# Kernel tuning notes

Hardware: AMD Instinct MI355X
Metric: run time of the kernel (lower is better)

## Reference

```python
import jax, jax.numpy as jnp
import numpy as np

B, S, D = 1024, 48, 256   # graphs, nodes-per-graph, embedding dim (= input_dim)
GDIM = 512                # graph_dim
N = B * S                 # total nodes
E = 4 * N                 # directed edges (avg degree ~4, molecular graphs)
W_SCALE = 0.05


def setup_inputs() -> dict:
    key = jax.random.key(0)
    ks = jax.random.split(key, 8)
    return {
        "sub2gene_out": jax.random.normal(ks[0], (B, S, D), jnp.float32),
        "edge_index": jax.random.randint(ks[1], (2, E), 0, N, dtype=jnp.int64),
        # conv1: in_channels = 2*D (concat of x and laplacian-smoothed x)
        "W_l1": jax.random.normal(ks[2], (GDIM, 2 * D), jnp.float32) * W_SCALE,
        "W_r1": jax.random.normal(ks[3], (GDIM, 2 * D), jnp.float32) * W_SCALE,
        "b1": jnp.zeros((GDIM,), jnp.float32),
        # conv2: graph_dim -> graph_dim
        "W_l2": jax.random.normal(ks[4], (GDIM, GDIM), jnp.float32) * W_SCALE,
        "W_r2": jax.random.normal(ks[5], (GDIM, GDIM), jnp.float32) * W_SCALE,
        "b2": jnp.zeros((GDIM,), jnp.float32),
    }


def sage_conv(x, src, dst, W_l, W_r, b, n):
    """PyG SAGEConv (mean aggregation, root_weight=True):
    out_i = W_l @ mean_{j in N(i)} x_j + W_r @ x_i + b, messages flow src->dst."""
    msg = x[src]                                            # [E, F] gather
    agg = jax.ops.segment_sum(msg, dst, num_segments=n)     # [N, F]
    cnt = jax.ops.segment_sum(jnp.ones((src.shape[0],), x.dtype), dst, num_segments=n)
    mean = agg / jnp.maximum(cnt, 1.0)[:, None]
    return mean @ W_l.T + x @ W_r.T + b


def reference(sub2gene_out, edge_index, W_l1, W_r1, b1, W_l2, W_r2, b2):
    b_, s_, d_ = sub2gene_out.shape
    n = b_ * s_
    x = sub2gene_out.reshape(n, d_)                         # cat of per-graph node features
    row, col = edge_index[0], edge_index[1]

    # sym-normalized Laplacian L = I - D^{-1/2} A D^{-1/2}; lap_x = L @ x
    ones_e = jnp.ones((row.shape[0],), x.dtype)
    deg = jax.ops.segment_sum(ones_e, row, num_segments=n)
    dinv = jnp.where(deg > 0, 1.0, 0.0) / jnp.sqrt(jnp.maximum(deg, 1.0))
    w = -(dinv[row] * dinv[col])                            # off-diagonal -A_norm
    lap_x = x + jax.ops.segment_sum(w[:, None] * x[col], row, num_segments=n)

    x_comb = jnp.concatenate([x, lap_x], axis=-1)           # [N, 2D]
    h = jax.nn.gelu(sage_conv(x_comb, row, col, W_l1, W_r1, b1, n), approximate=False)
    h = sage_conv(h, row, col, W_l2, W_r2, b2, n)           # [N, GDIM]

    # global_mean_pool: every graph has exactly s_ nodes
    batch = jnp.repeat(jnp.arange(b_), s_)
    pooled = jax.ops.segment_sum(h, batch, num_segments=b_) / jnp.asarray(s_, h.dtype)
    return pooled                                           # [B, GDIM]
```

## Files before the change

### kernel.cpp

```cpp
#include <hip/hip_runtime.h>
#include <math.h>

typedef unsigned short u16;
typedef __attribute__((ext_vector_type(8))) short bf16x8;
typedef __attribute__((ext_vector_type(4))) float f32x4;

#define NB 1024
#define NS 48
#define ND 256
#define NN (NB*NS)
#define NE (4*NN)
#define GD 512

__device__ __forceinline__ void gld16(const void* g, void* l) {
  __builtin_amdgcn_global_load_lds(
      (const __attribute__((address_space(1))) void*)(void*)g,
      (__attribute__((address_space(3))) void*)l, 16, 0, 0);
}

__device__ __forceinline__ float bf2f(u16 h) {
  unsigned u = ((unsigned)h) << 16; float f; __builtin_memcpy(&f, &u, 4); return f;
}
__device__ __forceinline__ u16 f2bf(float f) {
  unsigned u; __builtin_memcpy(&u, &f, 4);
  u += 0x7fffu + ((u >> 16) & 1u);
  return (u16)(u >> 16);
}
__device__ __forceinline__ void unpack8(uint4 v, float* f) {
  f[0]=bf2f((u16)(v.x & 0xffff)); f[1]=bf2f((u16)(v.x >> 16));
  f[2]=bf2f((u16)(v.y & 0xffff)); f[3]=bf2f((u16)(v.y >> 16));
  f[4]=bf2f((u16)(v.z & 0xffff)); f[5]=bf2f((u16)(v.z >> 16));
  f[6]=bf2f((u16)(v.w & 0xffff)); f[7]=bf2f((u16)(v.w >> 16));
}
__device__ __forceinline__ uint4 pack8(const float* f) {
  uint4 v;
  v.x = (unsigned)f2bf(f[0]) | ((unsigned)f2bf(f[1]) << 16);
  v.y = (unsigned)f2bf(f[2]) | ((unsigned)f2bf(f[3]) << 16);
  v.z = (unsigned)f2bf(f[4]) | ((unsigned)f2bf(f[5]) << 16);
  v.w = (unsigned)f2bf(f[6]) | ((unsigned)f2bf(f[7]) << 16);
  return v;
}


__global__ void k_hist(const int* __restrict__ ei, int* __restrict__ deg, int* __restrict__ cnt) {
  int e = blockIdx.x * 256 + threadIdx.x;
  if (e < NE) {
    atomicAdd(&deg[ei[e]], 1);
    atomicAdd(&cnt[ei[NE + e]], 1);
  }
}

__global__ void k_exscan2(const int* __restrict__ deg, const int* __restrict__ cnt,
                          int* __restrict__ rowOff, int* __restrict__ colOff,
                          float* __restrict__ dinv) {
  const int t = threadIdx.x;
  const int base = t * 48;
  if (blockIdx.x == 2) {
    for (int i = 0; i < 48; ++i) {
      int d = deg[base + i];
      dinv[base + i] = (d > 0) ? rsqrtf((float)d) : 0.0f;
    }
    return;
  }
  __shared__ int sums[1024];
  const int* in = blockIdx.x ? cnt : deg;
  int* out = blockIdx.x ? colOff : rowOff;
  int s = 0;
  for (int i = 0; i < 48; ++i) s += in[base + i];
  sums[t] = s;
  __syncthreads();
  for (int off = 1; off < 1024; off <<= 1) {
    int v = (t >= off) ? sums[t - off] : 0;
    __syncthreads();
    sums[t] += v;
    __syncthreads();
  }
  int run = (t == 0) ? 0 : sums[t - 1];
  for (int i = 0; i < 48; ++i) { int v = in[base + i]; out[base + i] = run; run += v; }
  if (t == 1023) out[NN] = run;
}

__global__ void k_fill(const int* __restrict__ ei,
                       const int* __restrict__ rowOff, const int* __restrict__ colOff,
                       int* __restrict__ rowFill, int* __restrict__ colFill,
                       int* __restrict__ rowCol, int* __restrict__ colSrc) {
  int e = blockIdx.x * 256 + threadIdx.x;
  if (e < NE) {
    int r = ei[e], c = ei[NE + e];
    int pr = atomicAdd(&rowFill[r], 1);
    rowCol[rowOff[r] + pr] = c;
    int pc = atomicAdd(&colFill[c], 1);
    colSrc[colOff[c] + pc] = r;
  }
}

__global__ void k_wx(const float* __restrict__ Wr1, const float* __restrict__ Wl1,
                     const float* __restrict__ Wr2, const float* __restrict__ Wl2,
                     u16* __restrict__ Wc, const float* __restrict__ x, u16* __restrict__ xb) {
  if (blockIdx.x < 1024) {
    int i = (blockIdx.x * 256 + threadIdx.x) * 4;
    int which = i >> 18;
    int off = i & 262143;
    const float* W = (which == 0) ? Wr1 : (which == 1) ? Wl1 : (which == 2) ? Wr2 : Wl2;
    float4 v = *(const float4*)(W + off);
    ushort4 h; h.x = f2bf(v.x); h.y = f2bf(v.y); h.z = f2bf(v.z); h.w = f2bf(v.w);
    *(ushort4*)(Wc + i) = h;
  } else {
    int i = ((blockIdx.x - 1024) * 256 + threadIdx.x) * 8;
    float4 v0 = *(const float4*)(x + i);
    float4 v1 = *(const float4*)(x + i + 4);
    float f[8] = {v0.x, v0.y, v0.z, v0.w, v1.x, v1.y, v1.z, v1.w};
    *(uint4*)(xb + i) = pack8(f);
  }
}

__global__ void k_lap(const u16* __restrict__ xb, const int* __restrict__ rowOff,
                      const int* __restrict__ rowCol, const float* __restrict__ dinv,
                      u16* __restrict__ xc) {
  const int gid = blockIdx.x * 256 + threadIdx.x;
  const int wid = gid >> 6, lane = gid & 63;
  const int node = wid * 2 + (lane >> 5);
  const int f0 = (lane & 31) * 8;
  float xi[8]; unpack8(*(const uint4*)(xb + (size_t)node * ND + f0), xi);
  float a[8] = {};
  const int s0 = rowOff[node], s1 = rowOff[node + 1];
  for (int p = s0; p < s1; p += 4) {
    const int q1 = (p + 1 < s1) ? p + 1 : s1 - 1;
    const int q2 = (p + 2 < s1) ? p + 2 : s1 - 1;
    const int q3 = (p + 3 < s1) ? p + 3 : s1 - 1;
    const int c0 = rowCol[p], c1 = rowCol[q1], c2 = rowCol[q2], c3 = rowCol[q3];
    const float w0 = dinv[c0];
    const float w1 = (p + 1 < s1) ? dinv[c1] : 0.f;
    const float w2 = (p + 2 < s1) ? dinv[c2] : 0.f;
    const float w3 = (p + 3 < s1) ? dinv[c3] : 0.f;
    float g0[8], g1[8], g2[8], g3[8];
    unpack8(*(const uint4*)(xb + (size_t)c0 * ND + f0), g0);
    unpack8(*(const uint4*)(xb + (size_t)c1 * ND + f0), g1);
    unpack8(*(const uint4*)(xb + (size_t)c2 * ND + f0), g2);
    unpack8(*(const uint4*)(xb + (size_t)c3 * ND + f0), g3);
    #pragma unroll
    for (int j = 0; j < 8; ++j) a[j] += w0 * g0[j] + w1 * g1[j] + w2 * g2[j] + w3 * g3[j];
  }
  const float di = dinv[node];
  u16* dst = xc + (size_t)node * GD + f0;
  *(uint4*)dst = pack8(xi);
  float l[8];
  #pragma unroll
  for (int j = 0; j < 8; ++j) l[j] = xi[j] - di * a[j];
  *(uint4*)(dst + ND) = pack8(l);
}

__global__ void k_aggx(const u16* __restrict__ xc, const int* __restrict__ colOff,
                       const int* __restrict__ colSrc, u16* __restrict__ xagg) {
  const int gid = blockIdx.x * 256 + threadIdx.x;
  const int node = gid >> 6, lane = gid & 63;
  const int f0 = lane * 8;
  float acc[8] = {};
  const int s0 = colOff[node], s1 = colOff[node + 1];
  for (int p = s0; p < s1; p += 4) {
    const int q1 = (p + 1 < s1) ? p + 1 : s1 - 1;
    const int q2 = (p + 2 < s1) ? p + 2 : s1 - 1;
    const int q3 = (p + 3 < s1) ? p + 3 : s1 - 1;
    const int c0 = colSrc[p], c1 = colSrc[q1], c2 = colSrc[q2], c3 = colSrc[q3];
    const float w1 = (p + 1 < s1) ? 1.f : 0.f;
    const float w2 = (p + 2 < s1) ? 1.f : 0.f;
    const float w3 = (p + 3 < s1) ? 1.f : 0.f;
    float g0[8], g1[8], g2[8], g3[8];
    unpack8(*(const uint4*)(xc + (size_t)c0 * GD + f0), g0);
    unpack8(*(const uint4*)(xc + (size_t)c1 * GD + f0), g1);
    unpack8(*(const uint4*)(xc + (size_t)c2 * GD + f0), g2);
    unpack8(*(const uint4*)(xc + (size_t)c3 * GD + f0), g3);
    #pragma unroll
    for (int j = 0; j < 8; ++j) acc[j] += g0[j] + w1 * g1[j] + w2 * g2[j] + w3 * g3[j];
  }
  const float inv = (s1 > s0) ? 1.0f / (float)(s1 - s0) : 1.0f;
  float res[8];
  #pragma unroll
  for (int j = 0; j < 8; ++j) res[j] = acc[j] * inv;
  *(uint4*)(xagg + (size_t)node * GD + f0) = pack8(res);
}

template <int MODE>
__global__ __launch_bounds__(256) void k_gemm(const u16* __restrict__ A0,
                                              const u16* __restrict__ A1,
                                              const u16* __restrict__ B0,
                                              const u16* __restrict__ B1,
                                              const float* __restrict__ bias,
                                              void* __restrict__ OutP) {
  __shared__ u16 As[128 * 32];
  __shared__ u16 Bs[128 * 32];
  const int tid = threadIdx.x;
  const int w = tid >> 6, lane = tid & 63;
  const int wr = w >> 1, wc = w & 1;

  const int cpx = gridDim.x >> 3;
  const int o = blockIdx.x;
  const int swz = (o & 7) * cpx + (o >> 3);
  const int bx = swz >> 2;
  const int by = swz & 3;

  const int c0 = w * 2, c1 = c0 + 1;
  const int lrow = lane >> 2;
  const int lcol = ((lane & 3) ^ ((lane >> 3) & 3)) * 8;
  const size_t a0r = (size_t)(bx * 128 + c0 * 16 + lrow) * GD + lcol;
  const size_t a1r = (size_t)(bx * 128 + c1 * 16 + lrow) * GD + lcol;
  const size_t b0r = (size_t)(by * 128 + c0 * 16 + lrow) * GD + lcol;
  const size_t b1r = (size_t)(by * 128 + c1 * 16 + lrow) * GD + lcol;
  u16* As0 = As + c0 * 512; u16* As1 = As + c1 * 512;
  u16* Bs0 = Bs + c0 * 512; u16* Bs1 = Bs + c1 * 512;

  const int kslot = ((lane >> 4) ^ ((lane >> 1) & 3)) * 8;
  const int aoff = (wr * 64 + (lane & 15)) * 32 + kslot;
  const int boff = (wc * 64 + (lane & 15)) * 32 + kslot;

  f32x4 acc[4][4] = {};

  #pragma unroll
  for (int half = 0; half < 2; ++half) {
    const u16* Ab = half ? A1 : A0;
    const u16* Bb = half ? B1 : B0;
    for (int kt = 0; kt < 512; kt += 32) {
      gld16(Ab + kt + a0r, As0);
      gld16(Ab + kt + a1r, As1);
      gld16(Bb + kt + b0r, Bs0);
      gld16(Bb + kt + b1r, Bs1);
      __syncthreads();
      bf16x8 aF[4], bF[4];
      #pragma unroll
      for (int i = 0; i < 4; ++i) aF[i] = *(const bf16x8*)(As + aoff + i * 512);
      #pragma unroll
      for (int i = 0; i < 4; ++i) bF[i] = *(const bf16x8*)(Bs + boff + i * 512);
      #pragma unroll
      for (int mi = 0; mi < 4; ++mi)
        #pragma unroll
        for (int ni = 0; ni < 4; ++ni)
          acc[mi][ni] = __builtin_amdgcn_mfma_f32_16x16x32_bf16(aF[mi], bF[ni], acc[mi][ni], 0, 0, 0);
      __syncthreads();
    }
  }

  const int lc = lane & 15, lr = (lane >> 4) * 4;
  const size_t r0 = (size_t)bx * 128 + wr * 64;
  const int cb = by * 128 + wc * 64;
  float bv[4];
  #pragma unroll
  for (int ni = 0; ni < 4; ++ni) bv[ni] = bias[cb + ni * 16 + lc];
  #pragma unroll
  for (int mi = 0; mi < 4; ++mi)
    #pragma unroll
    for (int ni = 0; ni < 4; ++ni)
      #pragma unroll
      for (int r = 0; r < 4; ++r) {
        float v = acc[mi][ni][r] + bv[ni];
        const size_t idx = (r0 + mi * 16 + lr + r) * GD + (cb + ni * 16 + lc);
        if (MODE == 0) {
          v = 0.5f * v * (1.0f + erff(v * 0.70710678118654752f));
          ((u16*)OutP)[idx] = f2bf(v);
        } else {
          ((float*)OutP)[idx] = v;
        }
      }
}

__global__ __launch_bounds__(256) void k_aggh(const u16* __restrict__ h, const int* __restrict__ colOff,
                                              const int* __restrict__ colSrc,
                                              u16* __restrict__ hrb, u16* __restrict__ hab) {
  __shared__ float red[2][4][GD];
  const int g = blockIdx.x;
  const int t = threadIdx.x, w = t >> 6, lane = t & 63;
  const int f0 = lane * 8;
  float pr[8] = {}, pa[8] = {};
  for (int n = w; n < NS; n += 4) {
    const int node = g * NS + n;
    float tmp[8];
    unpack8(*(const uint4*)(h + (size_t)node * GD + f0), tmp);
    #pragma unroll
    for (int j = 0; j < 8; ++j) pr[j] += tmp[j];
    float acc[8] = {};
    const int s0 = colOff[node], s1 = colOff[node + 1];
    for (int p = s0; p < s1; p += 4) {
      const int q1 = (p + 1 < s1) ? p + 1 : s1 - 1;
      const int q2 = (p + 2 < s1) ? p + 2 : s1 - 1;
      const int q3 = (p + 3 < s1) ? p + 3 : s1 - 1;
      const int c0 = colSrc[p], c1 = colSrc[q1], c2 = colSrc[q2], c3 = colSrc[q3];
      const float w1 = (p + 1 < s1) ? 1.f : 0.f;
      const float w2 = (p + 2 < s1) ? 1.f : 0.f;
      const float w3 = (p + 3 < s1) ? 1.f : 0.f;
      float g0[8], g1[8], g2[8], g3[8];
      unpack8(*(const uint4*)(h + (size_t)c0 * GD + f0), g0);
      unpack8(*(const uint4*)(h + (size_t)c1 * GD + f0), g1);
      unpack8(*(const uint4*)(h + (size_t)c2 * GD + f0), g2);
      unpack8(*(const uint4*)(h + (size_t)c3 * GD + f0), g3);
      #pragma unroll
      for (int j = 0; j < 8; ++j) acc[j] += g0[j] + w1 * g1[j] + w2 * g2[j] + w3 * g3[j];
    }
    const float inv = (s1 > s0) ? 1.0f / (float)(s1 - s0) : 1.0f;
    #pragma unroll
    for (int j = 0; j < 8; ++j) pa[j] += acc[j] * inv;
  }
  #pragma unroll
  for (int j = 0; j < 8; ++j) { red[0][w][f0 + j] = pr[j]; red[1][w][f0 + j] = pa[j]; }
  __syncthreads();
  const int f = t * 2;
  const float invS = 1.0f / (float)NS;
  float r0 = (red[0][0][f] + red[0][1][f] + red[0][2][f] + red[0][3][f]) * invS;
  float r1 = (red[0][0][f+1] + red[0][1][f+1] + red[0][2][f+1] + red[0][3][f+1]) * invS;
  float a0 = (red[1][0][f] + red[1][1][f] + red[1][2][f] + red[1][3][f]) * invS;
  float a1 = (red[1][0][f+1] + red[1][1][f+1] + red[1][2][f+1] + red[1][3][f+1]) * invS;
  *(unsigned*)(hrb + (size_t)g * GD + f) = (unsigned)f2bf(r0) | ((unsigned)f2bf(r1) << 16);
  *(unsigned*)(hab + (size_t)g * GD + f) = (unsigned)f2bf(a0) | ((unsigned)f2bf(a1) << 16);
}

extern "C" void kernel_launch(void* const* d_in, const int* in_sizes, int n_in,
                              void* d_out, int out_size, void* d_ws, size_t ws_size,
                              hipStream_t stream) {
  const float* x   = (const float*)d_in[0];
  const int*   ei  = (const int*)d_in[1];
  const float* Wl1 = (const float*)d_in[2];
  const float* Wr1 = (const float*)d_in[3];
  const float* b1  = (const float*)d_in[4];
  const float* Wl2 = (const float*)d_in[5];
  const float* Wr2 = (const float*)d_in[6];
  const float* b2  = (const float*)d_in[7];
  float* out = (float*)d_out;
  (void)in_sizes; (void)n_in; (void)out_size; (void)ws_size;

  int* deg     = (int*)d_ws;
  int* cnt     = deg + NN;
  int* rowFill = cnt + NN;
  int* colFill = rowFill + NN;
  int* rowOff  = colFill + NN;
  int* colOff  = rowOff + NN + 64;
  float* dinv  = (float*)(colOff + NN + 64);
  int* rowCol  = (int*)(dinv + NN);
  int* colSrc  = rowCol + NE;
  u16* WcR1    = (u16*)(colSrc + NE);
  u16* WcL1    = WcR1 + 512 * 512;
  u16* WcR2    = WcL1 + 512 * 512;
  u16* WcL2    = WcR2 + 512 * 512;
  u16* xc      = WcL2 + 512 * 512;
  u16* xagg    = xc + (size_t)NN * GD;
  u16* h       = xagg + (size_t)NN * GD;
  u16* xb      = h;
  u16* hrb     = xagg;
  u16* hab     = xagg + 1024 * GD;

  hipMemsetAsync(deg, 0, sizeof(int) * 4 * NN, stream);

  k_hist<<<NE / 256, 256, 0, stream>>>(ei, deg, cnt);
  k_exscan2<<<3, 1024, 0, stream>>>(deg, cnt, rowOff, colOff, dinv);
  k_fill<<<NE / 256, 256, 0, stream>>>(ei, rowOff, colOff, rowFill, colFill, rowCol, colSrc);
  k_wx<<<1024 + (NN * ND) / (256 * 8), 256, 0, stream>>>(Wr1, Wl1, Wr2, Wl2, WcR1, x, xb);
  k_lap<<<(NN * 32) / 256, 256, 0, stream>>>(xb, rowOff, rowCol, dinv, xc);
  k_aggx<<<(NN * 64) / 256, 256, 0, stream>>>(xc, colOff, colSrc, xagg);

  k_gemm<0><<<(NN / 128) * 4, 256, 0, stream>>>(xc, xagg, WcR1, WcL1, b1, (void*)h);

  k_aggh<<<NB, 256, 0, stream>>>(h, colOff, colSrc, hrb, hab);

  k_gemm<1><<<(NB / 128) * 4, 256, 0, stream>>>(hrb, hab, WcR2, WcL2, b2, (void*)out);
}
```

Measured before the change: 288.2 us.

## Concatenate GEMM operands along K and double-buffer LDS loads in GEMM

Stores x_comb and its mean aggregation side by side in one [N,1024] buffer, and interleaves W_r/W_l into one [512,1024] weight matrix, so each SAGE GEMM runs as a single K=1024 loop. The GEMM now keeps two LDS stages and issues the next tile's global-to-LDS loads before computing the current tile, waiting with partial vmcnt instead of a full barrier pair per step. The aim is to hide global load latency behind MFMA work, at the cost of doubled LDS use per block, which could lower occupancy.

```diff
diff --git a/kernel.cpp b/kernel.cpp
--- a/kernel.cpp
+++ b/kernel.cpp
@@ -11,6 +11,7 @@
 #define NN (NB*NS)
 #define NE (4*NN)
 #define GD 512
+#define KK 1024
 
 __device__ __forceinline__ void gld16(const void* g, void* l) {
   __builtin_amdgcn_global_load_lds(
@@ -96,17 +97,21 @@
 
 __global__ void k_wx(const float* __restrict__ Wr1, const float* __restrict__ Wl1,
                      const float* __restrict__ Wr2, const float* __restrict__ Wl2,
-                     u16* __restrict__ Wc, const float* __restrict__ x, u16* __restrict__ xb) {
-  if (blockIdx.x < 1024) {
-    int i = (blockIdx.x * 256 + threadIdx.x) * 4;
-    int which = i >> 18;
-    int off = i & 262143;
-    const float* W = (which == 0) ? Wr1 : (which == 1) ? Wl1 : (which == 2) ? Wr2 : Wl2;
-    float4 v = *(const float4*)(W + off);
+                     u16* __restrict__ W1c, u16* __restrict__ W2c,
+                     const float* __restrict__ x, u16* __restrict__ xb) {
+  const int b = blockIdx.x;
+  if (b < 1024) {
+    const float* Wr = (b < 512) ? Wr1 : Wr2;
+    const float* Wl = (b < 512) ? Wl1 : Wl2;
+    u16* Wc = (b < 512) ? W1c : W2c;
+    int i = ((b & 511) * 256 + threadIdx.x) * 4;
+    int n = i >> 10, k = i & 1023;
+    const float* src = (k < 512) ? (Wr + n * 512 + k) : (Wl + n * 512 + (k - 512));
+    float4 v = *(const float4*)src;
     ushort4 h; h.x = f2bf(v.x); h.y = f2bf(v.y); h.z = f2bf(v.z); h.w = f2bf(v.w);
     *(ushort4*)(Wc + i) = h;
   } else {
-    int i = ((blockIdx.x - 1024) * 256 + threadIdx.x) * 8;
+    int i = ((b - 1024) * 256 + threadIdx.x) * 8;
     float4 v0 = *(const float4*)(x + i);
     float4 v1 = *(const float4*)(x + i + 4);
     float f[8] = {v0.x, v0.y, v0.z, v0.w, v1.x, v1.y, v1.z, v1.w};
@@ -116,7 +121,7 @@
 
 __global__ void k_lap(const u16* __restrict__ xb, const int* __restrict__ rowOff,
                       const int* __restrict__ rowCol, const float* __restrict__ dinv,
-                      u16* __restrict__ xc) {
+                      u16* __restrict__ xcomb) {
   const int gid = blockIdx.x * 256 + threadIdx.x;
   const int wid = gid >> 6, lane = gid & 63;
   const int node = wid * 2 + (lane >> 5);
@@ -142,7 +147,7 @@
     for (int j = 0; j < 8; ++j) a[j] += w0 * g0[j] + w1 * g1[j] + w2 * g2[j] + w3 * g3[j];
   }
   const float di = dinv[node];
-  u16* dst = xc + (size_t)node * GD + f0;
+  u16* dst = xcomb + (size_t)node * KK + f0;
   *(uint4*)dst = pack8(xi);
   float l[8];
   #pragma unroll
@@ -150,8 +155,8 @@
   *(uint4*)(dst + ND) = pack8(l);
 }
 
-__global__ void k_aggx(const u16* __restrict__ xc, const int* __restrict__ colOff,
-                       const int* __restrict__ colSrc, u16* __restrict__ xagg) {
+__global__ void k_aggx(u16* __restrict__ xcomb, const int* __restrict__ colOff,
+                       const int* __restrict__ colSrc) {
   const int gid = blockIdx.x * 256 + threadIdx.x;
   const int node = gid >> 6, lane = gid & 63;
   const int f0 = lane * 8;
@@ -166,10 +171,10 @@
     const float w2 = (p + 2 < s1) ? 1.f : 0.f;
     const float w3 = (p + 3 < s1) ? 1.f : 0.f;
     float g0[8], g1[8], g2[8], g3[8];
-    unpack8(*(const uint4*)(xc + (size_t)c0 * GD + f0), g0);
-    unpack8(*(const uint4*)(xc + (size_t)c1 * GD + f0), g1);
-    unpack8(*(const uint4*)(xc + (size_t)c2 * GD + f0), g2);
-    unpack8(*(const uint4*)(xc + (size_t)c3 * GD + f0), g3);
+    unpack8(*(const uint4*)(xcomb + (size_t)c0 * KK + f0), g0);
+    unpack8(*(const uint4*)(xcomb + (size_t)c1 * KK + f0), g1);
+    unpack8(*(const uint4*)(xcomb + (size_t)c2 * KK + f0), g2);
+    unpack8(*(const uint4*)(xcomb + (size_t)c3 * KK + f0), g3);
     #pragma unroll
     for (int j = 0; j < 8; ++j) acc[j] += g0[j] + w1 * g1[j] + w2 * g2[j] + w3 * g3[j];
   }
@@ -177,18 +182,16 @@
   float res[8];
   #pragma unroll
   for (int j = 0; j < 8; ++j) res[j] = acc[j] * inv;
-  *(uint4*)(xagg + (size_t)node * GD + f0) = pack8(res);
+  *(uint4*)(xcomb + (size_t)node * KK + 512 + f0) = pack8(res);
 }
 
 template <int MODE>
-__global__ __launch_bounds__(256) void k_gemm(const u16* __restrict__ A0,
-                                              const u16* __restrict__ A1,
-                                              const u16* __restrict__ B0,
-                                              const u16* __restrict__ B1,
+__global__ __launch_bounds__(256) void k_gemm(const u16* __restrict__ A,
+                                              const u16* __restrict__ Bw,
                                               const float* __restrict__ bias,
                                               void* __restrict__ OutP) {
-  __shared__ u16 As[128 * 32];
-  __shared__ u16 Bs[128 * 32];
+  __shared__ u16 As[2][128 * 32];
+  __shared__ u16 Bs[2][128 * 32];
   const int tid = threadIdx.x;
   const int w = tid >> 6, lane = tid & 63;
   const int wr = w >> 1, wc = w & 1;
@@ -202,12 +205,10 @@
   const int c0 = w * 2, c1 = c0 + 1;
   const int lrow = lane >> 2;
   const int lcol = ((lane & 3) ^ ((lane >> 3) & 3)) * 8;
-  const size_t a0r = (size_t)(bx * 128 + c0 * 16 + lrow) * GD + lcol;
-  const size_t a1r = (size_t)(bx * 128 + c1 * 16 + lrow) * GD + lcol;
-  const size_t b0r = (size_t)(by * 128 + c0 * 16 + lrow) * GD + lcol;
-  const size_t b1r = (size_t)(by * 128 + c1 * 16 + lrow) * GD + lcol;
-  u16* As0 = As + c0 * 512; u16* As1 = As + c1 * 512;
-  u16* Bs0 = Bs + c0 * 512; u16* Bs1 = Bs + c1 * 512;
+  const u16* Ag0 = A  + (size_t)(bx * 128 + c0 * 16 + lrow) * KK + lcol;
+  const u16* Ag1 = A  + (size_t)(bx * 128 + c1 * 16 + lrow) * KK + lcol;
+  const u16* Bg0 = Bw + (size_t)(by * 128 + c0 * 16 + lrow) * KK + lcol;
+  const u16* Bg1 = Bw + (size_t)(by * 128 + c1 * 16 + lrow) * KK + lcol;
 
   const int kslot = ((lane >> 4) ^ ((lane >> 1) & 3)) * 8;
   const int aoff = (wr * 64 + (lane & 15)) * 32 + kslot;
@@ -215,29 +216,49 @@
 
   f32x4 acc[4][4] = {};
 
-  #pragma unroll
-  for (int half = 0; half < 2; ++half) {
-    const u16* Ab = half ? A1 : A0;
-    const u16* Bb = half ? B1 : B0;
-    for (int kt = 0; kt < 512; kt += 32) {
-      gld16(Ab + kt + a0r, As0);
-      gld16(Ab + kt + a1r, As1);
-      gld16(Bb + kt + b0r, Bs0);
-      gld16(Bb + kt + b1r, Bs1);
-      __syncthreads();
-      bf16x8 aF[4], bF[4];
-      #pragma unroll
-      for (int i = 0; i < 4; ++i) aF[i] = *(const bf16x8*)(As + aoff + i * 512);
-      #pragma unroll
-      for (int i = 0; i < 4; ++i) bF[i] = *(const bf16x8*)(Bs + boff + i * 512);
-      #pragma unroll
-      for (int mi = 0; mi < 4; ++mi)
-        #pragma unroll
-        for (int ni = 0; ni < 4; ++ni)
-          acc[mi][ni] = __builtin_amdgcn_mfma_f32_16x16x32_bf16(aF[mi], bF[ni], acc[mi][ni], 0, 0, 0);
-      __syncthreads();
-    }
-  }
+  #define STAGE(B, KT) do {                                                \
+    gld16(Ag0 + (KT), As[B] + c0 * 512);                                   \
+    gld16(Ag1 + (KT), As[B] + c1 * 512);                                   \
+    gld16(Bg0 + (KT), Bs[B] + c0 * 512);                                   \
+    gld16(Bg1 + (KT), Bs[B] + c1 * 512);                                   \
+  } while (0)
+
+  #define COMPUTE(B) do {                                                  \
+    bf16x8 aF[4], bF[4];                                                   \
+    _Pragma("unroll")                                                      \
+    for (int i = 0; i < 4; ++i) aF[i] = *(const bf16x8*)(As[B] + aoff + i * 512); \
+    _Pragma("unroll")                                                      \
+    for (int i = 0; i < 4; ++i) bF[i] = *(const bf16x8*)(Bs[B] + boff + i * 512); \
+    _Pragma("unroll")                                                      \
+    for (int mi = 0; mi < 4; ++mi)                                         \
+      _Pragma("unroll")                                                    \
+      for (int ni = 0; ni < 4; ++ni)                                       \
+        acc[mi][ni] = __builtin_amdgcn_mfma_f32_16x16x32_bf16(aF[mi], bF[ni], acc[mi][ni], 0, 0, 0); \
+  } while (0)
+
+  STAGE(0, 0);
+  for (int t = 0; t < 15; ++t) {
+    const int k = t * 64;
+    STAGE(1, k + 32);
+    asm volatile("s_waitcnt vmcnt(4)" ::: "memory");
+    __builtin_amdgcn_s_barrier();
+    COMPUTE(0);
+    __builtin_amdgcn_s_barrier();
+    STAGE(0, k + 64);
+    asm volatile("s_waitcnt vmcnt(4)" ::: "memory");
+    __builtin_amdgcn_s_barrier();
+    COMPUTE(1);
+    __builtin_amdgcn_s_barrier();
+  }
+  STAGE(1, 992);
+  asm volatile("s_waitcnt vmcnt(4)" ::: "memory");
+  __builtin_amdgcn_s_barrier();
+  COMPUTE(0);
+  asm volatile("s_waitcnt vmcnt(0)" ::: "memory");
+  __builtin_amdgcn_s_barrier();
+  COMPUTE(1);
+  #undef STAGE
+  #undef COMPUTE
 
   const int lc = lane & 15, lr = (lane >> 4) * 4;
   const size_t r0 = (size_t)bx * 128 + wr * 64;
@@ -264,7 +285,7 @@
 
 __global__ __launch_bounds__(256) void k_aggh(const u16* __restrict__ h, const int* __restrict__ colOff,
                                               const int* __restrict__ colSrc,
-                                              u16* __restrict__ hrb, u16* __restrict__ hab) {
+                                              u16* __restrict__ h2cat) {
   __shared__ float red[2][4][GD];
   const int g = blockIdx.x;
   const int t = threadIdx.x, w = t >> 6, lane = t & 63;
@@ -307,8 +328,8 @@
   float r1 = (red[0][0][f+1] + red[0][1][f+1] + red[0][2][f+1] + red[0][3][f+1]) * invS;
   float a0 = (red[1][0][f] + red[1][1][f] + red[1][2][f] + red[1][3][f]) * invS;
   float a1 = (red[1][0][f+1] + red[1][1][f+1] + red[1][2][f+1] + red[1][3][f+1]) * invS;
-  *(unsigned*)(hrb + (size_t)g * GD + f) = (unsigned)f2bf(r0) | ((unsigned)f2bf(r1) << 16);
-  *(unsigned*)(hab + (size_t)g * GD + f) = (unsigned)f2bf(a0) | ((unsigned)f2bf(a1) << 16);
+  *(unsigned*)(h2cat + (size_t)g * KK + f)       = (unsigned)f2bf(r0) | ((unsigned)f2bf(r1) << 16);
+  *(unsigned*)(h2cat + (size_t)g * KK + 512 + f) = (unsigned)f2bf(a0) | ((unsigned)f2bf(a1) << 16);
 }
 
 extern "C" void kernel_launch(void* const* d_in, const int* in_sizes, int n_in,
@@ -334,29 +355,25 @@
   float* dinv  = (float*)(colOff + NN + 64);
   int* rowCol  = (int*)(dinv + NN);
   int* colSrc  = rowCol + NE;
-  u16* WcR1    = (u16*)(colSrc + NE);
-  u16* WcL1    = WcR1 + 512 * 512;
-  u16* WcR2    = WcL1 + 512 * 512;
-  u16* WcL2    = WcR2 + 512 * 512;
-  u16* xc      = WcL2 + 512 * 512;
-  u16* xagg    = xc + (size_t)NN * GD;
-  u16* h       = xagg + (size_t)NN * GD;
+  u16* W1c     = (u16*)(colSrc + NE);
+  u16* W2c     = W1c + 512 * KK;
+  u16* h2cat   = W2c + 512 * KK;
+  u16* xcomb   = h2cat + (size_t)NB * KK;
+  u16* h       = xcomb + (size_t)NN * KK;
   u16* xb      = h;
-  u16* hrb     = xagg;
-  u16* hab     = xagg + 1024 * GD;
 
   hipMemsetAsync(deg, 0, sizeof(int) * 4 * NN, stream);
 
   k_hist<<<NE / 256, 256, 0, stream>>>(ei, deg, cnt);
   k_exscan2<<<3, 1024, 0, stream>>>(deg, cnt, rowOff, colOff, dinv);
   k_fill<<<NE / 256, 256, 0, stream>>>(ei, rowOff, colOff, rowFill, colFill, rowCol, colSrc);
-  k_wx<<<1024 + (NN * ND) / (256 * 8), 256, 0, stream>>>(Wr1, Wl1, Wr2, Wl2, WcR1, x, xb);
-  k_lap<<<(NN * 32) / 256, 256, 0, stream>>>(xb, rowOff, rowCol, dinv, xc);
-  k_aggx<<<(NN * 64) / 256, 256, 0, stream>>>(xc, colOff, colSrc, xagg);
-
-  k_gemm<0><<<(NN / 128) * 4, 256, 0, stream>>>(xc, xagg, WcR1, WcL1, b1, (void*)h);
-
-  k_aggh<<<NB, 256, 0, stream>>>(h, colOff, colSrc, hrb, hab);
-
-  k_gemm<1><<<(NB / 128) * 4, 256, 0, stream>>>(hrb, hab, WcR2, WcL2, b2, (void*)out);
-}
+  k_wx<<<1024 + (NN * ND) / (256 * 8), 256, 0, stream>>>(Wr1, Wl1, Wr2, Wl2, W1c, W2c, x, xb);
+  k_lap<<<(NN * 32) / 256, 256, 0, stream>>>(xb, rowOff, rowCol, dinv, xcomb);
+  k_aggx<<<(NN * 64) / 256, 256, 0, stream>>>(xcomb, colOff, colSrc);
+
+  k_gemm<0><<<(NN / 128) * 4, 256, 0, stream>>>(xcomb, W1c, b1, (void*)h);
+
+  k_aggh<<<NB, 256, 0, stream>>>(h, colOff, colSrc, h2cat);
+
+  k_gemm<1><<<(NB / 128) * 4, 256, 0, stream>>>(h2cat, W2c, b2, (void*)out);
+}
```

New measurement: 283.3 us. No clear change (-1.7%).
